# Kernel tuning notes

Hardware: AMD Instinct MI355X
Metric: run time of the kernel (lower is better)

Reference implementation:

```python
import jax, jax.numpy as jnp
import numpy as np


def setup_inputs() -> dict:
    key = jax.random.key(0)
    k1, k2, k3, k4 = jax.random.split(key, 4)
    B, S, D = 4, 2048, 1024
    return {
        "x": jax.random.normal(k1, (B, S, D), dtype=jnp.float32),
        "wq": jax.random.normal(k2, (D, D), dtype=jnp.float32),
        "wk": jax.random.normal(k3, (D, D), dtype=jnp.float32),
        "wv": jax.random.normal(k4, (D, D), dtype=jnp.float32),
    }


def reference(x, wq, wk, wv):
    # q,k,v: [B,S,D]
    q = x @ wq
    k = x @ wk
    v = x @ wv
    # NOTE: source applies NO 1/sqrt(d) scaling; we match it faithfully.
    scores = jnp.einsum("bsd,btd->bst", q, k)  # [B,S,S]
    weights = jax.nn.softmax(scores, axis=-1)
    return jnp.einsum("bst,btd->bsd", weights, v)  # [B,S,D]
```

## Files before the change

kernel.cpp:

```cpp
#include <hip/hip_runtime.h>


typedef _Float16 half4_t __attribute__((ext_vector_type(4)));
typedef _Float16 half8_t __attribute__((ext_vector_type(8)));
typedef float f32x4 __attribute__((ext_vector_type(4)));

#define BM 128
#define BN 128
#define BK 32

__device__ __forceinline__ void gl_lds16(const _Float16* g, _Float16* l) {
    __builtin_amdgcn_global_load_lds(
        (const __attribute__((address_space(1))) unsigned int*)g,
        (__attribute__((address_space(3))) unsigned int*)l, 16, 0, 0);
}

__global__ __launch_bounds__(256) void conv_all_kernel(
    const float* __restrict__ x, const float* __restrict__ wq,
    const float* __restrict__ wk, const float* __restrict__ wv,
    _Float16* __restrict__ xh, _Float16* __restrict__ xl,
    _Float16* __restrict__ qh, _Float16* __restrict__ ql,
    _Float16* __restrict__ kh, _Float16* __restrict__ kl,
    _Float16* __restrict__ vTh)
{
    __shared__ float tle[64][65];
    const int bid = blockIdx.x;
    if (bid < 10240) {
        const float* in;
        _Float16 *hi, *lo;
        int i0;
        if (bid < 8192)      { in = x;  hi = xh; lo = xl; i0 = bid; }
        else if (bid < 9216) { in = wq; hi = qh; lo = ql; i0 = bid - 8192; }
        else                 { in = wk; hi = kh; lo = kl; i0 = bid - 9216; }
        int i = i0 * 256 + threadIdx.x;
        float4 v = ((const float4*)in)[i];
        float xs[4] = {v.x, v.y, v.z, v.w};
        half4_t h, l;
#pragma unroll
        for (int j = 0; j < 4; ++j) {
            _Float16 hh = (_Float16)xs[j];
            h[j] = hh;
            l[j] = (_Float16)(xs[j] - (float)hh);
        }
        ((half4_t*)hi)[i] = h;
        ((half4_t*)lo)[i] = l;
    } else {
        const int t = bid - 10240;
        const int tr = (t >> 4) * 64, tc = (t & 15) * 64;
        const int t16 = threadIdx.x & 15, tq = threadIdx.x >> 4;
#pragma unroll
        for (int j = 0; j < 4; ++j) {
            int lr = tq + j * 16;
            float4 v = *(const float4*)(wv + (size_t)(tr + lr) * 1024 + tc + t16 * 4);
            tle[lr][t16 * 4 + 0] = v.x;
            tle[lr][t16 * 4 + 1] = v.y;
            tle[lr][t16 * 4 + 2] = v.z;
            tle[lr][t16 * 4 + 3] = v.w;
        }
        __syncthreads();
#pragma unroll
        for (int j = 0; j < 4; ++j) {
            int orow = tq + j * 16;
            int oc = t16 * 4;
            half4_t h;
#pragma unroll
            for (int i = 0; i < 4; ++i) h[i] = (_Float16)tle[oc + i][orow];
            *(half4_t*)(vTh + (size_t)(tc + orow) * 1024 + tr + oc) = h;
        }
    }
}

template <bool OUTF32>
__global__ __launch_bounds__(256) void gemm_split(
    const _Float16* __restrict__ Ah, const _Float16* __restrict__ Al, size_t az,
    const _Float16* __restrict__ Bh, const _Float16* __restrict__ Bl, size_t bz,
    float* __restrict__ Cf, size_t cz, int ldc,
    _Float16* __restrict__ Oh, _Float16* __restrict__ Ol, size_t oz, int ldo,
    int lda, int ldb, int K)
{
    __shared__ __align__(16) _Float16 sAh[BM][BK], sAl[BM][BK];
    __shared__ __align__(16) _Float16 sBh[BN][BK], sBl[BN][BK];

    const int tid = threadIdx.x;
    const int wave = tid >> 6, lane = tid & 63;
    const int wm = (wave >> 1) * 64, wn = (wave & 1) * 64;
    const int lrow = lane & 15, quad = lane >> 4;
    const int bm = blockIdx.y * BM, bn = blockIdx.x * BN;
    const int z = blockIdx.z;

    const _Float16* pAh = Ah + (size_t)z * az;
    const _Float16* pAl = Al + (size_t)z * az;
    const _Float16* pBh = Bh + (size_t)z * bz;
    const _Float16* pBl = Bl + (size_t)z * bz;

    const int r0 = wave * 32 + (lane >> 2);
    const int kofs = (lane & 3) * 8;
    const size_t a0o = (size_t)(bm + r0) * lda + kofs;
    const size_t a1o = a0o + (size_t)16 * lda;
    const size_t b0o = (size_t)(bn + r0) * ldb + kofs;
    const size_t b1o = b0o + (size_t)16 * ldb;
    _Float16* lA0 = &sAh[r0][kofs];
    _Float16* lA1 = &sAh[r0 + 16][kofs];
    _Float16* lAl0 = &sAl[r0][kofs];
    _Float16* lAl1 = &sAl[r0 + 16][kofs];
    _Float16* lB0 = &sBh[r0][kofs];
    _Float16* lB1 = &sBh[r0 + 16][kofs];
    _Float16* lBl0 = &sBl[r0][kofs];
    _Float16* lBl1 = &sBl[r0 + 16][kofs];

    f32x4 acc[4][4];
#pragma unroll
    for (int i = 0; i < 4; ++i)
#pragma unroll
        for (int j = 0; j < 4; ++j) acc[i][j] = 0.0f;

    for (int k0 = 0; k0 < K; k0 += BK) {
        gl_lds16(pAh + a0o + k0, lA0);
        gl_lds16(pAh + a1o + k0, lA1);
        gl_lds16(pAl + a0o + k0, lAl0);
        gl_lds16(pAl + a1o + k0, lAl1);
        gl_lds16(pBh + b0o + k0, lB0);
        gl_lds16(pBh + b1o + k0, lB1);
        gl_lds16(pBl + b0o + k0, lBl0);
        gl_lds16(pBl + b1o + k0, lBl1);
        __syncthreads();

        half8_t a0[4], a1[4], b0[4], b1[4];
#pragma unroll
        for (int mt = 0; mt < 4; ++mt) {
            a0[mt] = *(const half8_t*)&sAh[wm + mt * 16 + lrow][quad * 8];
            a1[mt] = *(const half8_t*)&sAl[wm + mt * 16 + lrow][quad * 8];
        }
#pragma unroll
        for (int nt = 0; nt < 4; ++nt) {
            b0[nt] = *(const half8_t*)&sBh[wn + nt * 16 + lrow][quad * 8];
            b1[nt] = *(const half8_t*)&sBl[wn + nt * 16 + lrow][quad * 8];
        }
#pragma unroll
        for (int mt = 0; mt < 4; ++mt)
#pragma unroll
            for (int nt = 0; nt < 4; ++nt) {
                acc[mt][nt] = __builtin_amdgcn_mfma_f32_16x16x32_f16(a0[mt], b0[nt], acc[mt][nt], 0, 0, 0);
                acc[mt][nt] = __builtin_amdgcn_mfma_f32_16x16x32_f16(a0[mt], b1[nt], acc[mt][nt], 0, 0, 0);
                acc[mt][nt] = __builtin_amdgcn_mfma_f32_16x16x32_f16(a1[mt], b0[nt], acc[mt][nt], 0, 0, 0);
            }
        __syncthreads();
    }

#pragma unroll
    for (int mt = 0; mt < 4; ++mt)
#pragma unroll
        for (int nt = 0; nt < 4; ++nt)
#pragma unroll
            for (int r = 0; r < 4; ++r) {
                int gm = bm + wm + mt * 16 + quad * 4 + r;
                int gn = bn + wn + nt * 16 + lrow;
                float v = acc[mt][nt][r];
                if (OUTF32) {
                    Cf[(size_t)z * cz + (size_t)gm * ldc + gn] = v;
                } else {
                    _Float16 h = (_Float16)v;
                    Oh[(size_t)z * oz + (size_t)gm * ldo + gn] = h;
                    Ol[(size_t)z * oz + (size_t)gm * ldo + gn] = (_Float16)(v - (float)h);
                }
            }
}

#define NSTEPS 96

__global__ __launch_bounds__(1024) void scores_16w(
    const _Float16* __restrict__ yh, const _Float16* __restrict__ yl,
    const _Float16* __restrict__ xh, const _Float16* __restrict__ xl,
    float* __restrict__ Cf)
{
    __shared__ __align__(16) _Float16 sA[2][8192];
    __shared__ __align__(16) _Float16 sB[2][8192];

    const int tid = threadIdx.x;
    const int wave = tid >> 6, lane = tid & 63;
    const int wm = (wave >> 2) * 64;
    const int wn = (wave & 3) * 64;
    const int l15 = lane & 15, jq = lane >> 4;

    const int flat = blockIdx.x + (blockIdx.y << 3) + (blockIdx.z << 6);
    const int work = ((flat & 7) << 5) + (flat >> 3);
    const int z = work >> 6;
    const int bm = ((work >> 3) & 7) * 256;
    const int bn = (work & 7) * 256;

    const _Float16* Ah = yh + ((size_t)z * 2048 + bm) * 1024;
    const _Float16* Al = yl + ((size_t)z * 2048 + bm) * 1024;
    const _Float16* Bh = xh + ((size_t)z * 2048 + bn) * 1024;
    const _Float16* Bl = xl + ((size_t)z * 2048 + bn) * 1024;

    int a_off0, b_off0;
    {
        int row = wm + l15;
        a_off0 = (row * 4 + (jq ^ ((row >> 1) & 3))) * 16;
        row = wn + l15;
        b_off0 = (row * 4 + (jq ^ ((row >> 1) & 3))) * 16;
    }
    int row0 = tid >> 2;
    int j0 = (tid & 3) ^ ((row0 >> 1) & 3);
    int g0 = row0 * 2048 + j0 * 16;
    int wb0 = tid * 16;

    f32x4 rA, rB;

    auto ISSUE = [&](const _Float16* pa, const _Float16* pb) {
        rA = *(const f32x4*)((const char*)pa + g0);
        rB = *(const f32x4*)((const char*)pb + g0);
    };
    auto WRITE = [&](_Float16* slotA, _Float16* slotB) {
        *(f32x4*)((char*)slotA + wb0) = rA;
        *(f32x4*)((char*)slotB + wb0) = rB;
    };
    auto APAN = [&](int t) { return (t < 64 ? Ah : Al) + (t & 31) * 32; };
    auto BPAN = [&](int t) { return (((t >> 5) == 1) ? Bl : Bh) + (t & 31) * 32; };

    f32x4 acc[4][4];
#pragma unroll
    for (int i = 0; i < 4; ++i)
#pragma unroll
        for (int j = 0; j < 4; ++j) acc[i][j] = 0.0f;

    auto STEP = [&](const _Float16* sa, const _Float16* sb,
                    _Float16* wa, _Float16* wb, int tn) {
        half8_t fa[4], fb[4];
#pragma unroll
        for (int m = 0; m < 4; ++m)
            fa[m] = *(const half8_t*)((const char*)sa + a_off0 + m * 1024);
#pragma unroll
        for (int n = 0; n < 4; ++n)
            fb[n] = *(const half8_t*)((const char*)sb + b_off0 + n * 1024);
        WRITE(wa, wb);
        ISSUE(APAN(tn), BPAN(tn));
        __builtin_amdgcn_s_setprio(1);
#pragma unroll
        for (int m = 0; m < 4; ++m)
#pragma unroll
            for (int n = 0; n < 4; ++n)
                acc[m][n] = __builtin_amdgcn_mfma_f32_16x16x32_f16(
                    fa[m], fb[n], acc[m][n], 0, 0, 0);
        __builtin_amdgcn_s_setprio(0);
        __builtin_amdgcn_s_barrier();
    };

    ISSUE(APAN(0), BPAN(0));
    WRITE(sA[0], sB[0]);
    ISSUE(APAN(1), BPAN(1));
    __syncthreads();

    for (int t = 0; t < NSTEPS; t += 2) {
        const int t2 = (t + 2 < NSTEPS) ? t + 2 : NSTEPS - 1;
        const int t3 = (t + 3 < NSTEPS) ? t + 3 : NSTEPS - 1;
        STEP(sA[0], sB[0], sA[1], sB[1], t2);
        STEP(sA[1], sB[1], sA[0], sB[0], t3);
    }

    float* C = Cf + (size_t)z * 2048 * 2048;
#pragma unroll
    for (int mi = 0; mi < 4; ++mi)
#pragma unroll
        for (int ni = 0; ni < 4; ++ni) {
            int gm0 = bm + wm + mi * 16 + jq * 4;
            int gn = bn + wn + ni * 16 + l15;
#pragma unroll
            for (int r = 0; r < 4; ++r)
                C[(size_t)(gm0 + r) * 2048 + gn] = acc[mi][ni][r];
        }
}

__global__ __launch_bounds__(256) void yv_kernel(
    const _Float16* __restrict__ xh, const _Float16* __restrict__ xl,
    const _Float16* __restrict__ Mh, const _Float16* __restrict__ Ml,
    const _Float16* __restrict__ wvTh,
    _Float16* __restrict__ yh, _Float16* __restrict__ yl,
    _Float16* __restrict__ vT)
{
    __shared__ __align__(16) char buf[128 * 132 * 2];

    const int tid = threadIdx.x;
    const int wave = tid >> 6, lane = tid & 63;
    const int wm = (wave >> 1) * 64, wn = (wave & 1) * 64;
    const int lrow = lane & 15, quad = lane >> 4;
    const int bm = blockIdx.y * BM, bn = blockIdx.x * BN;
    const bool vrole = (blockIdx.z != 0);

    const int r0 = wave * 32 + (lane >> 2);
    const int kofs = (lane & 3) * 8;
    const size_t a0o = (size_t)(bm + r0) * 1024 + kofs;
    const size_t a1o = a0o + (size_t)16 * 1024;
    const size_t b0o = (size_t)(bn + r0) * 1024 + kofs;
    const size_t b1o = b0o + (size_t)16 * 1024;

    f32x4 acc[4][4];
#pragma unroll
    for (int i = 0; i < 4; ++i)
#pragma unroll
        for (int j = 0; j < 4; ++j) acc[i][j] = 0.0f;

    _Float16* tle = (_Float16*)buf;

    if (!vrole) {
        _Float16* sAh = (_Float16*)buf;
        _Float16* sAl = (_Float16*)(buf + 8192);
        _Float16* sBh = (_Float16*)(buf + 16384);
        _Float16* sBl = (_Float16*)(buf + 24576);
        _Float16* lA0 = sAh + r0 * BK + kofs;
        _Float16* lA1 = sAh + (r0 + 16) * BK + kofs;
        _Float16* lAl0 = sAl + r0 * BK + kofs;
        _Float16* lAl1 = sAl + (r0 + 16) * BK + kofs;
        _Float16* lB0 = sBh + r0 * BK + kofs;
        _Float16* lB1 = sBh + (r0 + 16) * BK + kofs;
        _Float16* lBl0 = sBl + r0 * BK + kofs;
        _Float16* lBl1 = sBl + (r0 + 16) * BK + kofs;

        for (int k0 = 0; k0 < 1024; k0 += BK) {
            gl_lds16(xh + a0o + k0, lA0);
            gl_lds16(xh + a1o + k0, lA1);
            gl_lds16(xl + a0o + k0, lAl0);
            gl_lds16(xl + a1o + k0, lAl1);
            gl_lds16(Mh + b0o + k0, lB0);
            gl_lds16(Mh + b1o + k0, lB1);
            gl_lds16(Ml + b0o + k0, lBl0);
            gl_lds16(Ml + b1o + k0, lBl1);
            __syncthreads();

            half8_t a0[4], a1[4], b0[4], b1[4];
#pragma unroll
            for (int mt = 0; mt < 4; ++mt) {
                a0[mt] = *(const half8_t*)(sAh + (wm + mt * 16 + lrow) * BK + quad * 8);
                a1[mt] = *(const half8_t*)(sAl + (wm + mt * 16 + lrow) * BK + quad * 8);
            }
#pragma unroll
            for (int nt = 0; nt < 4; ++nt) {
                b0[nt] = *(const half8_t*)(sBh + (wn + nt * 16 + lrow) * BK + quad * 8);
                b1[nt] = *(const half8_t*)(sBl + (wn + nt * 16 + lrow) * BK + quad * 8);
            }
#pragma unroll
            for (int mt = 0; mt < 4; ++mt)
#pragma unroll
                for (int nt = 0; nt < 4; ++nt) {
                    acc[mt][nt] = __builtin_amdgcn_mfma_f32_16x16x32_f16(a0[mt], b0[nt], acc[mt][nt], 0, 0, 0);
                    acc[mt][nt] = __builtin_amdgcn_mfma_f32_16x16x32_f16(a0[mt], b1[nt], acc[mt][nt], 0, 0, 0);
                    acc[mt][nt] = __builtin_amdgcn_mfma_f32_16x16x32_f16(a1[mt], b0[nt], acc[mt][nt], 0, 0, 0);
                }
            __syncthreads();
        }

#pragma unroll
        for (int pass = 0; pass < 2; ++pass) {
            if (pass) __syncthreads();
#pragma unroll
            for (int mt = 0; mt < 4; ++mt)
#pragma unroll
                for (int nt = 0; nt < 4; ++nt) {
                    int rloc = wm + mt * 16 + quad * 4;
                    int cloc = wn + nt * 16 + lrow;
#pragma unroll
                    for (int r = 0; r < 4; ++r) {
                        float v = acc[mt][nt][r];
                        _Float16 h = (_Float16)v;
                        tle[(rloc + r) * 132 + cloc] =
                            pass == 0 ? h : (_Float16)(v - (float)h);
                    }
                }
            __syncthreads();
            _Float16* dst = pass == 0 ? yh : yl;
#pragma unroll
            for (int i = 0; i < 8; ++i) {
                int flat = i * 256 + tid;
                int rloc = flat >> 4, c = (flat & 15) * 8;
                half8_t o8;
#pragma unroll
                for (int j = 0; j < 8; ++j) o8[j] = tle[rloc * 132 + c + j];
                *(half8_t*)(dst + (size_t)(bm + rloc) * 1024 + bn + c) = o8;
            }
        }
    } else {
        _Float16* sA = (_Float16*)buf;
        _Float16* sB = (_Float16*)(buf + 8192);
        _Float16* lA0 = sA + r0 * BK + kofs;
        _Float16* lA1 = sA + (r0 + 16) * BK + kofs;
        _Float16* lB0 = sB + r0 * BK + kofs;
        _Float16* lB1 = sB + (r0 + 16) * BK + kofs;

        for (int k0 = 0; k0 < 1024; k0 += BK) {
            gl_lds16(xh + a0o + k0, lA0);
            gl_lds16(xh + a1o + k0, lA1);
            gl_lds16(wvTh + b0o + k0, lB0);
            gl_lds16(wvTh + b1o + k0, lB1);
            __syncthreads();

            half8_t a0[4], b0[4];
#pragma unroll
            for (int mt = 0; mt < 4; ++mt)
                a0[mt] = *(const half8_t*)(sA + (wm + mt * 16 + lrow) * BK + quad * 8);
#pragma unroll
            for (int nt = 0; nt < 4; ++nt)
                b0[nt] = *(const half8_t*)(sB + (wn + nt * 16 + lrow) * BK + quad * 8);
#pragma unroll
            for (int mt = 0; mt < 4; ++mt)
#pragma unroll
                for (int nt = 0; nt < 4; ++nt)
                    acc[mt][nt] = __builtin_amdgcn_mfma_f32_16x16x32_f16(a0[mt], b0[nt], acc[mt][nt], 0, 0, 0);
            __syncthreads();
        }

#pragma unroll
        for (int mt = 0; mt < 4; ++mt)
#pragma unroll
            for (int nt = 0; nt < 4; ++nt) {
                int t0 = wm + mt * 16 + quad * 4;
                int e_l = wn + nt * 16 + lrow;
                half4_t o;
#pragma unroll
                for (int r = 0; r < 4; ++r) o[r] = (_Float16)acc[mt][nt][r];
                *(half4_t*)(tle + e_l * 132 + t0) = o;
            }
        __syncthreads();
        const int b = bm >> 11, tb = bm & 2047;
#pragma unroll
        for (int i = 0; i < 8; ++i) {
            int flat = i * 256 + tid;
            int e_l = flat >> 4, c = (flat & 15) * 8;
            half8_t o8;
#pragma unroll
            for (int j = 0; j < 8; ++j) o8[j] = tle[e_l * 132 + c + j];
            *(half8_t*)(vT + ((size_t)b << 21) + (size_t)(bn + e_l) * 2048 + tb + c) = o8;
        }
    }
}

__global__ __launch_bounds__(256) void gemm_plain(
    const _Float16* __restrict__ Ag, size_t az,
    const _Float16* __restrict__ Bg, size_t bz,
    float* __restrict__ Cf, size_t cz, int ldc,
    int lda, int ldb, int K)
{
    __shared__ __align__(16) _Float16 sA[BM][BK], sB[BN][BK];

    const int tid = threadIdx.x;
    const int wave = tid >> 6, lane = tid & 63;
    const int wm = (wave >> 1) * 64, wn = (wave & 1) * 64;
    const int lrow = lane & 15, quad = lane >> 4;
    const int bm = blockIdx.y * BM, bn = blockIdx.x * BN;
    const int z = blockIdx.z;

    const _Float16* pA = Ag + (size_t)z * az;
    const _Float16* pB = Bg + (size_t)z * bz;

    const int r0 = wave * 32 + (lane >> 2);
    const int kofs = (lane & 3) * 8;
    const size_t a0o = (size_t)(bm + r0) * lda + kofs;
    const size_t a1o = a0o + (size_t)16 * lda;
    const size_t b0o = (size_t)(bn + r0) * ldb + kofs;
    const size_t b1o = b0o + (size_t)16 * ldb;
    _Float16* lA0 = &sA[r0][kofs];
    _Float16* lA1 = &sA[r0 + 16][kofs];
    _Float16* lB0 = &sB[r0][kofs];
    _Float16* lB1 = &sB[r0 + 16][kofs];

    f32x4 acc[4][4];
#pragma unroll
    for (int i = 0; i < 4; ++i)
#pragma unroll
        for (int j = 0; j < 4; ++j) acc[i][j] = 0.0f;

    for (int k0 = 0; k0 < K; k0 += BK) {
        gl_lds16(pA + a0o + k0, lA0);
        gl_lds16(pA + a1o + k0, lA1);
        gl_lds16(pB + b0o + k0, lB0);
        gl_lds16(pB + b1o + k0, lB1);
        __syncthreads();

        half8_t a0[4], b0[4];
#pragma unroll
        for (int mt = 0; mt < 4; ++mt)
            a0[mt] = *(const half8_t*)&sA[wm + mt * 16 + lrow][quad * 8];
#pragma unroll
        for (int nt = 0; nt < 4; ++nt)
            b0[nt] = *(const half8_t*)&sB[wn + nt * 16 + lrow][quad * 8];
#pragma unroll
        for (int mt = 0; mt < 4; ++mt)
#pragma unroll
            for (int nt = 0; nt < 4; ++nt)
                acc[mt][nt] = __builtin_amdgcn_mfma_f32_16x16x32_f16(a0[mt], b0[nt], acc[mt][nt], 0, 0, 0);
        __syncthreads();
    }

#pragma unroll
    for (int mt = 0; mt < 4; ++mt)
#pragma unroll
        for (int nt = 0; nt < 4; ++nt) {
            int gm0 = bm + wm + mt * 16 + quad * 4;
            int gn = bn + wn + nt * 16 + lrow;
#pragma unroll
            for (int r = 0; r < 4; ++r)
                Cf[(size_t)z * cz + (size_t)(gm0 + r) * ldc + gn] = acc[mt][nt][r];
        }
}

__global__ __launch_bounds__(256) void softmax_kernel(float* __restrict__ S)
{
    float* row = S + (size_t)blockIdx.x * 2048;
    float4* r4 = (float4*)row;
    const int tid = threadIdx.x;
    const int wave = tid >> 6, lane = tid & 63;

    float4 a = r4[tid], b = r4[tid + 256];
    float m = fmaxf(fmaxf(fmaxf(a.x, a.y), fmaxf(a.z, a.w)),
                    fmaxf(fmaxf(b.x, b.y), fmaxf(b.z, b.w)));
#pragma unroll
    for (int o = 32; o; o >>= 1) m = fmaxf(m, __shfl_xor(m, o));
    __shared__ float redm[4];
    __shared__ float reds[4];
    if (lane == 0) redm[wave] = m;
    __syncthreads();
    m = fmaxf(fmaxf(redm[0], redm[1]), fmaxf(redm[2], redm[3]));

    a.x = __expf(a.x - m); a.y = __expf(a.y - m);
    a.z = __expf(a.z - m); a.w = __expf(a.w - m);
    b.x = __expf(b.x - m); b.y = __expf(b.y - m);
    b.z = __expf(b.z - m); b.w = __expf(b.w - m);

    float s = a.x + a.y + a.z + a.w + b.x + b.y + b.z + b.w;
#pragma unroll
    for (int o = 32; o; o >>= 1) s += __shfl_xor(s, o);
    if (lane == 0) reds[wave] = s;
    __syncthreads();
    s = reds[0] + reds[1] + reds[2] + reds[3];

    float inv = 1.0f / s;
    _Float16* o16 = (_Float16*)row;
    half4_t ha, hb;
    ha[0] = (_Float16)(a.x * inv); ha[1] = (_Float16)(a.y * inv);
    ha[2] = (_Float16)(a.z * inv); ha[3] = (_Float16)(a.w * inv);
    hb[0] = (_Float16)(b.x * inv); hb[1] = (_Float16)(b.y * inv);
    hb[2] = (_Float16)(b.z * inv); hb[3] = (_Float16)(b.w * inv);
    ((half4_t*)o16)[tid] = ha;
    ((half4_t*)o16)[tid + 256] = hb;
}

extern "C" void kernel_launch(void* const* d_in, const int* in_sizes, int n_in,
                              void* d_out, int out_size, void* d_ws, size_t ws_size,
                              hipStream_t stream)
{
    const float* x  = (const float*)d_in[0];
    const float* wq = (const float*)d_in[1];
    const float* wk = (const float*)d_in[2];
    const float* wv = (const float*)d_in[3];
    float* out = (float*)d_out;

    const int S = 2048, D = 1024;
    char* ws = (char*)d_ws;

    _Float16* xh   = (_Float16*)(ws);
    _Float16* xl   = (_Float16*)(ws + (16ull << 20));
    _Float16* yh   = (_Float16*)(ws + (32ull << 20));
    _Float16* yl   = (_Float16*)(ws + (48ull << 20));
    _Float16* vT   = (_Float16*)(ws + (64ull << 20));
    _Float16* wqh  = (_Float16*)(ws + (80ull << 20));
    _Float16* wql  = (_Float16*)(ws + (82ull << 20));
    _Float16* wkh  = (_Float16*)(ws + (84ull << 20));
    _Float16* wkl  = (_Float16*)(ws + (86ull << 20));
    _Float16* wvTh = (_Float16*)(ws + (88ull << 20));
    _Float16* Mh   = (_Float16*)(ws + (90ull << 20));
    _Float16* Ml   = (_Float16*)(ws + (92ull << 20));
    float*    sc   = (float*)(ws + (94ull << 20));

    conv_all_kernel<<<dim3(10496), dim3(256), 0, stream>>>(
        x, wq, wk, wv, xh, xl, wqh, wql, wkh, wkl, wvTh);

    gemm_split<false><<<dim3(D / BN, D / BM, 1), dim3(256), 0, stream>>>(
        wkh, wkl, 0, wqh, wql, 0, nullptr, 0, 0, Mh, Ml, 0, D, D, D, D);

    yv_kernel<<<dim3(D / BN, 8192 / BM, 2), dim3(256), 0, stream>>>(
        xh, xl, Mh, Ml, wvTh, yh, yl, vT);

    scores_16w<<<dim3(S / 256, S / 256, 4), dim3(1024), 0, stream>>>(
        yh, yl, xh, xl, sc);

    softmax_kernel<<<dim3(4 * S), dim3(256), 0, stream>>>(sc);

    gemm_plain<<<dim3(D / BN, S / BM, 4), dim3(256), 0, stream>>>(
        (const _Float16*)sc, (size_t)S * 4096, vT, (size_t)D * S,
        out, (size_t)S * D, D, 4096, S, S);
}
```

Measured before the change: 406.2 us.

## Restructure scores kernel to 8 waves with 128x64 warp tiles and fused split-fp16 loads

The scores kernel goes from 16 waves per 1024-thread block to 8 waves with two blocks per CU. Each wave now computes a 128x64 tile. Instead of streaming the three split-precision products (hh, hl, lh) as 96 sequential K panels, each K step loads the high and low halves of A and B together and issues all three MFMAs per fragment pair, so there are 32 steps. The aim is to cut redundant panel reloads and barrier count and to raise MFMA density per LDS read, at the cost of twice the LDS footprint (64 KB), more accumulator registers and more global loads in flight per thread.

```diff
diff --git a/kernel.cpp b/kernel.cpp
--- a/kernel.cpp
+++ b/kernel.cpp
@@ -166,19 +166,19 @@
             }
 }
 
-#define NSTEPS 96
-
-__global__ __launch_bounds__(1024) void scores_16w(
+#define NSTEPS 32
+
+__global__ __launch_bounds__(512, 2) void scores_c3(
     const _Float16* __restrict__ yh, const _Float16* __restrict__ yl,
     const _Float16* __restrict__ xh, const _Float16* __restrict__ xl,
     float* __restrict__ Cf)
 {
-    __shared__ __align__(16) _Float16 sA[2][8192];
-    __shared__ __align__(16) _Float16 sB[2][8192];
+    __shared__ __align__(16) _Float16 sAh[2][8192], sAl[2][8192];
+    __shared__ __align__(16) _Float16 sBh[2][8192], sBl[2][8192];
 
     const int tid = threadIdx.x;
     const int wave = tid >> 6, lane = tid & 63;
-    const int wm = (wave >> 2) * 64;
+    const int wm = (wave >> 2) * 128;
     const int wn = (wave & 3) * 64;
     const int l15 = lane & 15, jq = lane >> 4;
 
@@ -200,67 +200,83 @@
         row = wn + l15;
         b_off0 = (row * 4 + (jq ^ ((row >> 1) & 3))) * 16;
     }
+    asm volatile("" : "+v"(a_off0), "+v"(b_off0));
     int row0 = tid >> 2;
     int j0 = (tid & 3) ^ ((row0 >> 1) & 3);
     int g0 = row0 * 2048 + j0 * 16;
+    int g1 = g0 + 262144;
     int wb0 = tid * 16;
-
-    f32x4 rA, rB;
-
-    auto ISSUE = [&](const _Float16* pa, const _Float16* pb) {
-        rA = *(const f32x4*)((const char*)pa + g0);
-        rB = *(const f32x4*)((const char*)pb + g0);
+    asm volatile("" : "+v"(g0), "+v"(g1), "+v"(wb0));
+
+    f32x4 rAh[2], rAl[2], rBh[2], rBl[2];
+
+    auto ISSUE = [&](int t) {
+        const char* pa = (const char*)(Ah + t * 32);
+        const char* pl = (const char*)(Al + t * 32);
+        const char* pb = (const char*)(Bh + t * 32);
+        const char* pq = (const char*)(Bl + t * 32);
+        rAh[0] = *(const f32x4*)(pa + g0); rAh[1] = *(const f32x4*)(pa + g1);
+        rAl[0] = *(const f32x4*)(pl + g0); rAl[1] = *(const f32x4*)(pl + g1);
+        rBh[0] = *(const f32x4*)(pb + g0); rBh[1] = *(const f32x4*)(pb + g1);
+        rBl[0] = *(const f32x4*)(pq + g0); rBl[1] = *(const f32x4*)(pq + g1);
     };
-    auto WRITE = [&](_Float16* slotA, _Float16* slotB) {
-        *(f32x4*)((char*)slotA + wb0) = rA;
-        *(f32x4*)((char*)slotB + wb0) = rB;
+    auto WRITE = [&](int p) {
+        *(f32x4*)((char*)sAh[p] + wb0) = rAh[0];
+        *(f32x4*)((char*)sAh[p] + wb0 + 8192) = rAh[1];
+        *(f32x4*)((char*)sAl[p] + wb0) = rAl[0];
+        *(f32x4*)((char*)sAl[p] + wb0 + 8192) = rAl[1];
+        *(f32x4*)((char*)sBh[p] + wb0) = rBh[0];
+        *(f32x4*)((char*)sBh[p] + wb0 + 8192) = rBh[1];
+        *(f32x4*)((char*)sBl[p] + wb0) = rBl[0];
+        *(f32x4*)((char*)sBl[p] + wb0 + 8192) = rBl[1];
     };
-    auto APAN = [&](int t) { return (t < 64 ? Ah : Al) + (t & 31) * 32; };
-    auto BPAN = [&](int t) { return (((t >> 5) == 1) ? Bl : Bh) + (t & 31) * 32; };
-
-    f32x4 acc[4][4];
-#pragma unroll
-    for (int i = 0; i < 4; ++i)
+
+    f32x4 acc[8][4];
+#pragma unroll
+    for (int i = 0; i < 8; ++i)
 #pragma unroll
         for (int j = 0; j < 4; ++j) acc[i][j] = 0.0f;
 
-    auto STEP = [&](const _Float16* sa, const _Float16* sb,
-                    _Float16* wa, _Float16* wb, int tn) {
-        half8_t fa[4], fb[4];
-#pragma unroll
-        for (int m = 0; m < 4; ++m)
-            fa[m] = *(const half8_t*)((const char*)sa + a_off0 + m * 1024);
-#pragma unroll
-        for (int n = 0; n < 4; ++n)
-            fb[n] = *(const half8_t*)((const char*)sb + b_off0 + n * 1024);
-        WRITE(wa, wb);
-        ISSUE(APAN(tn), BPAN(tn));
+    auto STEP = [&](int p, int tn) {
+        half8_t bhf[4], blf[4];
+#pragma unroll
+        for (int n = 0; n < 4; ++n) {
+            bhf[n] = *(const half8_t*)((const char*)sBh[p] + b_off0 + n * 1024);
+            blf[n] = *(const half8_t*)((const char*)sBl[p] + b_off0 + n * 1024);
+        }
+        WRITE(p ^ 1);
+        ISSUE(tn);
         __builtin_amdgcn_s_setprio(1);
 #pragma unroll
-        for (int m = 0; m < 4; ++m)
-#pragma unroll
-            for (int n = 0; n < 4; ++n)
-                acc[m][n] = __builtin_amdgcn_mfma_f32_16x16x32_f16(
-                    fa[m], fb[n], acc[m][n], 0, 0, 0);
+        for (int m = 0; m < 8; ++m) {
+            half8_t ahf = *(const half8_t*)((const char*)sAh[p] + a_off0 + m * 1024);
+            half8_t alf = *(const half8_t*)((const char*)sAl[p] + a_off0 + m * 1024);
+#pragma unroll
+            for (int n = 0; n < 4; ++n) {
+                acc[m][n] = __builtin_amdgcn_mfma_f32_16x16x32_f16(ahf, bhf[n], acc[m][n], 0, 0, 0);
+                acc[m][n] = __builtin_amdgcn_mfma_f32_16x16x32_f16(ahf, blf[n], acc[m][n], 0, 0, 0);
+                acc[m][n] = __builtin_amdgcn_mfma_f32_16x16x32_f16(alf, bhf[n], acc[m][n], 0, 0, 0);
+            }
+        }
         __builtin_amdgcn_s_setprio(0);
         __builtin_amdgcn_s_barrier();
     };
 
-    ISSUE(APAN(0), BPAN(0));
-    WRITE(sA[0], sB[0]);
-    ISSUE(APAN(1), BPAN(1));
+    ISSUE(0);
+    WRITE(0);
+    ISSUE(1);
     __syncthreads();
 
-    for (int t = 0; t < NSTEPS; t += 2) {
-        const int t2 = (t + 2 < NSTEPS) ? t + 2 : NSTEPS - 1;
-        const int t3 = (t + 3 < NSTEPS) ? t + 3 : NSTEPS - 1;
-        STEP(sA[0], sB[0], sA[1], sB[1], t2);
-        STEP(sA[1], sB[1], sA[0], sB[0], t3);
+    for (int s = 0; s < NSTEPS; s += 2) {
+        const int t2 = (s + 2 < NSTEPS) ? s + 2 : NSTEPS - 1;
+        const int t3 = (s + 3 < NSTEPS) ? s + 3 : NSTEPS - 1;
+        STEP(0, t2);
+        STEP(1, t3);
     }
 
     float* C = Cf + (size_t)z * 2048 * 2048;
 #pragma unroll
-    for (int mi = 0; mi < 4; ++mi)
+    for (int mi = 0; mi < 8; ++mi)
 #pragma unroll
         for (int ni = 0; ni < 4; ++ni) {
             int gm0 = bm + wm + mi * 16 + jq * 4;
@@ -579,7 +595,7 @@
     yv_kernel<<<dim3(D / BN, 8192 / BM, 2), dim3(256), 0, stream>>>(
         xh, xl, Mh, Ml, wvTh, yh, yl, vT);
 
-    scores_16w<<<dim3(S / 256, S / 256, 4), dim3(1024), 0, stream>>>(
+    scores_c3<<<dim3(S / 256, S / 256, 4), dim3(512), 0, stream>>>(
         yh, yl, xh, xl, sc);
 
     softmax_kernel<<<dim3(4 * S), dim3(256), 0, stream>>>(sc);
```

Result: faster. 387.9 us (-4.5%).
